# Optimization experiments

Hardware: AMD Instinct MI355X
Metric: run time of the kernel (lower is better)

## Reference

```python
import jax, jax.numpy as jnp
import numpy as np

N = 4096
F_IN = 512
F_OUT = 64
HEADS = 8
ALPHA = 0.2  # LeakyReLU negative slope
NEG_INF = -9e15


def setup_inputs() -> dict:
    key = jax.random.key(0)
    k1, k2, k3, k4 = jax.random.split(key, 4)
    x = jax.random.normal(k1, (N, F_IN), dtype=jnp.float32)
    adj = jax.random.randint(k2, (N, N), 0, 2, dtype=jnp.int32)  # dense 0/1 adjacency
    # xavier_uniform with gain=1.414 per head
    limW = 1.414 * float(np.sqrt(6.0 / (F_IN + F_OUT)))
    lima = 1.414 * float(np.sqrt(6.0 / (2 * F_OUT + 1)))
    W = jax.random.uniform(k3, (HEADS, F_IN, F_OUT), minval=-limW, maxval=limW, dtype=jnp.float32)
    a = jax.random.uniform(k4, (HEADS, 2 * F_OUT), minval=-lima, maxval=lima, dtype=jnp.float32)
    return {"x": x, "adj": adj, "W": W, "a": a}


def reference(x, adj, W, a):
    # Per-head linear: Wh [H, N, F_OUT]
    Wh = jnp.einsum("nf,hfo->hno", x, W)
    # Pairwise concat + matmul with a decomposes into f1_i + f2_j
    f1 = jnp.einsum("hno,ho->hn", Wh, a[:, :F_OUT])  # [H, N]
    f2 = jnp.einsum("hno,ho->hn", Wh, a[:, F_OUT:])  # [H, N]
    e = jax.nn.leaky_relu(f1[:, :, None] + f2[:, None, :], ALPHA)  # [H, N, N]
    e = jnp.where(adj[None, :, :] > 0, e, NEG_INF)
    attn = jax.nn.softmax(e, axis=-1)  # masked row softmax; dropout is eval-mode identity
    out = jnp.einsum("hnm,hmo->hno", attn, Wh)  # weighted aggregation
    # concat heads: [N, H*F_OUT]
    return jnp.transpose(out, (1, 0, 2)).reshape(N, HEADS * F_OUT)
```

## Files before the change

### kernel.cpp

```cpp
#include <hip/hip_runtime.h>
#include <hip/hip_bf16.h>

#define NN   4096
#define FIN  512
#define FOUT 64
#define NH   8
#define ALPHA 0.2f
#define ROWS 128
#define LOG2E 1.4426950408889634f

typedef __attribute__((ext_vector_type(8))) short bf16x8;
typedef __attribute__((ext_vector_type(4))) float f32x4;

__device__ __forceinline__ unsigned short f2bf(float x) {
    unsigned u = __float_as_uint(x);
    return (unsigned short)((u + 0x7fffu + ((u >> 16) & 1u)) >> 16);
}

__device__ __forceinline__ unsigned pk2(float a, float b) {
    union { __hip_bfloat162 h2; unsigned u; } cv;
    cv.h2 = __float22bfloat162_rn(float2{a, b});
    return cv.u;
}

__global__ __launch_bounds__(256) void kb(const int* __restrict__ adj,
                                          unsigned long long* __restrict__ bits) {
    const int wv   = blockIdx.x * 4 + (threadIdx.x >> 6);
    const int lane = threadIdx.x & 63;
    const int base = wv * 32;
    #pragma unroll
    for (int r = 0; r < 4; ++r) {
        int v0 = adj[(size_t)(base + r*8 + 0) * 64 + lane];
        int v1 = adj[(size_t)(base + r*8 + 1) * 64 + lane];
        int v2 = adj[(size_t)(base + r*8 + 2) * 64 + lane];
        int v3 = adj[(size_t)(base + r*8 + 3) * 64 + lane];
        int v4 = adj[(size_t)(base + r*8 + 4) * 64 + lane];
        int v5 = adj[(size_t)(base + r*8 + 5) * 64 + lane];
        int v6 = adj[(size_t)(base + r*8 + 6) * 64 + lane];
        int v7 = adj[(size_t)(base + r*8 + 7) * 64 + lane];
        unsigned long long m0 = __ballot(v0 > 0);
        unsigned long long m1 = __ballot(v1 > 0);
        unsigned long long m2 = __ballot(v2 > 0);
        unsigned long long m3 = __ballot(v3 > 0);
        unsigned long long m4 = __ballot(v4 > 0);
        unsigned long long m5 = __ballot(v5 > 0);
        unsigned long long m6 = __ballot(v6 > 0);
        unsigned long long m7 = __ballot(v7 > 0);
        if (lane == 0) {
            ulonglong2* dst = (ulonglong2*)&bits[base + r*8];
            dst[0] = {m0, m1};
            dst[1] = {m2, m3};
            dst[2] = {m4, m5};
            dst[3] = {m6, m7};
        }
    }
}

__global__ __launch_bounds__(256) void kg(const float* __restrict__ x,
                                          const float* __restrict__ W,
                                          const float* __restrict__ aw,
                                          unsigned short* __restrict__ WhTs,
                                          float* __restrict__ f1,
                                          float* __restrict__ f2) {
    __shared__ float As[16][68];
    __shared__ float Bs[16][68];
    __shared__ unsigned short Tb[64][80];
    __shared__ float r1[64][16];
    __shared__ float r2[64][16];
    const int t = threadIdx.x;
    const int bx   = blockIdx.x;
    const int h    = bx >> 6;
    const int nti  = bx & 63;
    const int row0 = nti * 64;
    const int tr = t >> 4, tc = t & 15;
    const int ar = t >> 2, ak = t & 3;
    const int bk = t >> 4, bo = t & 15;
    const float* WH = W + (size_t)h * FIN * FOUT;
    float acc[4][4] = {};

    for (int k0i = 0; k0i < FIN; k0i += 16) {
        __syncthreads();
        float4 av = *(const float4*)&x[(size_t)(row0 + ar) * FIN + k0i + ak * 4];
        As[ak*4+0][ar] = av.x; As[ak*4+1][ar] = av.y;
        As[ak*4+2][ar] = av.z; As[ak*4+3][ar] = av.w;
        *(float4*)&Bs[bk][bo*4] =
            *(const float4*)&WH[(size_t)(k0i + bk) * FOUT + bo*4];
        __syncthreads();
        #pragma unroll
        for (int kk = 0; kk < 16; ++kk) {
            float4 a4 = *(const float4*)&As[kk][tr*4];
            float4 b4 = *(const float4*)&Bs[kk][tc*4];
            float a[4] = {a4.x, a4.y, a4.z, a4.w};
            float b[4] = {b4.x, b4.y, b4.z, b4.w};
            #pragma unroll
            for (int i = 0; i < 4; ++i)
                #pragma unroll
                for (int j = 0; j < 4; ++j)
                    acc[i][j] = fmaf(a[i], b[j], acc[i][j]);
        }
    }

    float a1v[4], a2v[4];
    #pragma unroll
    for (int j = 0; j < 4; ++j) {
        a1v[j] = aw[h * 2 * FOUT + tc*4 + j];
        a2v[j] = aw[h * 2 * FOUT + FOUT + tc*4 + j];
    }
    #pragma unroll
    for (int i = 0; i < 4; ++i) {
        float s1 = 0.f, s2 = 0.f;
        #pragma unroll
        for (int j = 0; j < 4; ++j) {
            s1 = fmaf(acc[i][j], a1v[j], s1);
            s2 = fmaf(acc[i][j], a2v[j], s2);
            Tb[tc*4 + j][tr*4 + i] = f2bf(acc[i][j]);
        }
        r1[tr*4 + i][tc] = s1;
        r2[tr*4 + i][tc] = s2;
    }
    __syncthreads();
    if (t < 64) {
        float s1 = 0.f, s2 = 0.f;
        #pragma unroll
        for (int k = 0; k < 16; ++k) { s1 += r1[t][k]; s2 += r2[t][k]; }
        f1[h * NN + row0 + t] = s1 * LOG2E;
        f2[h * NN + row0 + t] = s2 * LOG2E;
    }
    unsigned char* tileB = (unsigned char*)(WhTs + ((size_t)(h * 64) + nti) * 4096);
    #pragma unroll
    for (int i = 0; i < 2; ++i) {
        int c = t + i * 256;
        int o = c >> 3, nch = c & 7;
        *(uint4*)(tileB + o * 128 + ((nch * 16) ^ ((o & 7) << 4))) =
            *(const uint4*)&Tb[o][nch * 8];
    }
}

__global__ __launch_bounds__(256, 4) void k3_attn(
        const unsigned long long* __restrict__ bits,
        const unsigned short* __restrict__ WhTs,
        const float* __restrict__ f1, const float* __restrict__ f2,
        float* __restrict__ pnum, float* __restrict__ pden) {
    __shared__ unsigned char psB[ROWS * 128];
    __shared__ unsigned char wsB[8192];
    const int t    = threadIdx.x;
    const int lane = t & 63, wid = t >> 6;
    const int h    = blockIdx.y;
    const int row0 = blockIdx.x * ROWS;
    const int js   = blockIdx.z, JS = gridDim.z;
    const int ntile = (NN / 64) / JS;
    const int nt0   = js * ntile;
    const int pr   = t >> 1, psub = t & 1;
    const float f1r = f1[h * NN + row0 + pr];
    const float* f2h = f2 + h * NN;
    const unsigned long long* bitsRow = bits + (size_t)(row0 + pr) * 64;
    const unsigned short* WTS = WhTs + (size_t)h * 64 * 4096;
    const int prswz = (pr & 7) << 4;
    f32x4 acc[2][4] = {};
    f32x4 accd[2] = {};
    const bf16x8 ones = {0x3F80, 0x3F80, 0x3F80, 0x3F80,
                         0x3F80, 0x3F80, 0x3F80, 0x3F80};

    uint4 wreg0, wreg1;
    auto loadW = [&](int nti, uint4& w0, uint4& w1) {
        const uint4* gt = (const uint4*)(WTS + (size_t)nti * 4096);
        w0 = gt[t];
        w1 = gt[t + 256];
    };
    loadW(nt0, wreg0, wreg1);

    const int kb2 = (lane >> 4) * 16;
    for (int it = 0; it < ntile; ++it) {
        const int nti = nt0 + it;
        __syncthreads();
        *(uint4*)&wsB[t * 16]        = wreg0;
        *(uint4*)&wsB[t * 16 + 4096] = wreg1;
        {
            unsigned msk = (unsigned)(bitsRow[nti] >> (psub << 5));
            const float* f2c = f2h + nti * 64 + psub * 32;
            #pragma unroll
            for (int q = 0; q < 4; ++q) {
                unsigned pk[4];
                #pragma unroll
                for (int c2 = 0; c2 < 2; ++c2) {
                    float4 f4 = *(const float4*)&f2c[q * 8 + c2 * 4];
                    float e0 = f1r + f4.x, e1 = f1r + f4.y;
                    float e2 = f1r + f4.z, e3 = f1r + f4.w;
                    e0 = fmaxf(e0, ALPHA * e0); e1 = fmaxf(e1, ALPHA * e1);
                    e2 = fmaxf(e2, ALPHA * e2); e3 = fmaxf(e3, ALPHA * e3);
                    const int b = q * 8 + c2 * 4;
                    float p0 = ((msk >> (b+0)) & 1u) ? __builtin_amdgcn_exp2f(e0) : 0.f;
                    float p1 = ((msk >> (b+1)) & 1u) ? __builtin_amdgcn_exp2f(e1) : 0.f;
                    float p2 = ((msk >> (b+2)) & 1u) ? __builtin_amdgcn_exp2f(e2) : 0.f;
                    float p3 = ((msk >> (b+3)) & 1u) ? __builtin_amdgcn_exp2f(e3) : 0.f;
                    pk[c2*2+0] = pk2(p0, p1);
                    pk[c2*2+1] = pk2(p2, p3);
                }
                uint4 w = {pk[0], pk[1], pk[2], pk[3]};
                *(uint4*)&psB[pr * 128 + ((psub*64 + q*16) ^ prswz)] = w;
            }
        }
        if (it + 1 < ntile) loadW(nti + 1, wreg0, wreg1);
        __syncthreads();
        #pragma unroll
        for (int fg = 0; fg < 2; ++fg) {
            const int arw  = wid * 32 + fg * 16 + (lane & 15);
            const int aswz = (arw & 7) << 4;
            #pragma unroll
            for (int ks = 0; ks < 2; ++ks) {
                bf16x8 af = *(const bf16x8*)&psB[arw * 128 + ((ks*64 + kb2) ^ aswz)];
                accd[fg] = __builtin_amdgcn_mfma_f32_16x16x32_bf16(af, ones, accd[fg], 0, 0, 0);
                #pragma unroll
                for (int cf = 0; cf < 4; ++cf) {
                    int brw = cf * 16 + (lane & 15);
                    bf16x8 bfr = *(const bf16x8*)&wsB[brw * 128 + ((ks*64 + kb2) ^ ((brw & 7) << 4))];
                    acc[fg][cf] = __builtin_amdgcn_mfma_f32_16x16x32_bf16(af, bfr, acc[fg][cf], 0, 0, 0);
                }
            }
        }
    }

    float* pn = pnum + (((size_t)js * NH + h) * NN + row0) * 64;
    #pragma unroll
    for (int fg = 0; fg < 2; ++fg)
        #pragma unroll
        for (int cf = 0; cf < 4; ++cf) {
            int o = cf * 16 + (lane & 15);
            #pragma unroll
            for (int rg = 0; rg < 4; ++rg) {
                int rl = wid * 32 + fg * 16 + (lane >> 4) * 4 + rg;
                pn[(size_t)rl * 64 + o] = acc[fg][cf][rg];
            }
        }
    if ((lane & 15) == 0) {
        float* pd = pden + ((size_t)js * NH + h) * NN + row0;
        #pragma unroll
        for (int fg = 0; fg < 2; ++fg)
            #pragma unroll
            for (int rg = 0; rg < 4; ++rg)
                pd[wid * 32 + fg * 16 + (lane >> 4) * 4 + rg] = accd[fg][rg];
    }
}

__global__ __launch_bounds__(256) void k4_red(const float* __restrict__ pnum,
                                              const float* __restrict__ pden,
                                              float* __restrict__ out, int JS) {
    const int idx = blockIdx.x * 256 + threadIdx.x;
    const int h   = idx >> 16;
    const int rem = idx & 65535;
    const int n   = rem >> 4;
    const int o4  = (rem & 15) * 4;
    float4 s = {0.f, 0.f, 0.f, 0.f};
    float  d = 0.f;
    for (int js = 0; js < JS; ++js) {
        const float* p = pnum + (((size_t)js * NH + h) * NN + n) * 64 + o4;
        float4 v = *(const float4*)p;
        s.x += v.x; s.y += v.y; s.z += v.z; s.w += v.w;
        d += pden[((size_t)js * NH + h) * NN + n];
    }
    float inv = 1.0f / d;
    float4 r = {s.x * inv, s.y * inv, s.z * inv, s.w * inv};
    *(float4*)&out[(size_t)n * (NH * FOUT) + h * FOUT + o4] = r;
}

extern "C" void kernel_launch(void* const* d_in, const int* in_sizes, int n_in,
                              void* d_out, int out_size, void* d_ws, size_t ws_size,
                              hipStream_t stream) {
    const float* x   = (const float*)d_in[0];
    const int*   adj = (const int*)d_in[1];
    const float* W   = (const float*)d_in[2];
    const float* a   = (const float*)d_in[3];
    float* outp = (float*)d_out;

    unsigned short* WhTs = (unsigned short*)d_ws;
    float* f1 = (float*)(WhTs + (size_t)NH * 64 * NN);
    float* f2 = f1 + NH * NN;
    unsigned long long* bits = (unsigned long long*)(f2 + NH * NN);
    float* pnum = (float*)(bits + (size_t)NN * 64);
    const size_t baseBytes  = (size_t)(pnum - (float*)d_ws) * 4;
    const size_t sliceBytes = (size_t)NH * NN * 65 * 4;
    int JS = 1;
    if (ws_size >= baseBytes + 4 * sliceBytes) JS = 4;
    else if (ws_size >= baseBytes + 2 * sliceBytes) JS = 2;
    float* pden = pnum + (size_t)JS * NH * NN * 64;

    kb     <<<dim3(2048),            256, 0, stream>>>(adj, bits);
    kg     <<<dim3(512),             256, 0, stream>>>(x, W, a, WhTs, f1, f2);
    k3_attn<<<dim3(NN/ROWS, NH, JS), 256, 0, stream>>>(bits, WhTs, f1, f2, pnum, pden);
    k4_red <<<dim3(NN*NH*FOUT/4/256), 256, 0, stream>>>(pnum, pden, outp, JS);
}
```

Baseline: 109.6 us.

## Use bf16 MFMA for the Wh projection with a pre-transposed bf16 W

Replaces the scalar fp32 shared-memory GEMM in kg with bf16 MFMA 16x16x32 instructions. A new small kernel kw first converts W to bf16 and transposes it so each lane can load contiguous 8-element B fragments. x is converted to bf16 on the fly and read directly from global memory without LDS staging. This adds one extra kernel launch and lowers the projection precision to bf16 inputs, which also affects f1/f2.

```diff
diff --git a/kernel.cpp b/kernel.cpp
--- a/kernel.cpp
+++ b/kernel.cpp
@@ -21,6 +21,10 @@
     union { __hip_bfloat162 h2; unsigned u; } cv;
     cv.h2 = __float22bfloat162_rn(float2{a, b});
     return cv.u;
+}
+
+__device__ __forceinline__ bf16x8 u4bf8(uint4 u) {
+    union { uint4 a; bf16x8 b; } cv; cv.a = u; return cv.b;
 }
 
 __global__ __launch_bounds__(256) void kb(const int* __restrict__ adj,
@@ -56,67 +60,81 @@
     }
 }
 
+__global__ __launch_bounds__(256) void kw(const float* __restrict__ W,
+                                          unsigned short* __restrict__ WT) {
+    __shared__ unsigned short T[64][72];
+    const int t  = threadIdx.x;
+    const int h  = blockIdx.x >> 3;
+    const int k0 = (blockIdx.x & 7) * 64;
+    #pragma unroll
+    for (int i = 0; i < 4; ++i) {
+        int idx = t + i * 256;
+        int kk = idx >> 4, o4 = (idx & 15) * 4;
+        float4 v = *(const float4*)&W[((size_t)h * FIN + k0 + kk) * FOUT + o4];
+        T[o4+0][kk] = f2bf(v.x); T[o4+1][kk] = f2bf(v.y);
+        T[o4+2][kk] = f2bf(v.z); T[o4+3][kk] = f2bf(v.w);
+    }
+    __syncthreads();
+    #pragma unroll
+    for (int i = 0; i < 2; ++i) {
+        int c = t + i * 256;
+        int o = c >> 3, kch = (c & 7) * 8;
+        *(uint4*)&WT[((size_t)h * 64 + o) * FIN + k0 + kch] =
+            *(const uint4*)&T[o][kch];
+    }
+}
+
 __global__ __launch_bounds__(256) void kg(const float* __restrict__ x,
-                                          const float* __restrict__ W,
+                                          const unsigned short* __restrict__ WT,
                                           const float* __restrict__ aw,
                                           unsigned short* __restrict__ WhTs,
                                           float* __restrict__ f1,
                                           float* __restrict__ f2) {
-    __shared__ float As[16][68];
-    __shared__ float Bs[16][68];
     __shared__ unsigned short Tb[64][80];
     __shared__ float r1[64][16];
     __shared__ float r2[64][16];
-    const int t = threadIdx.x;
-    const int bx   = blockIdx.x;
-    const int h    = bx >> 6;
-    const int nti  = bx & 63;
+    const int t = threadIdx.x, lane = t & 63, wid = t >> 6;
+    const int h    = blockIdx.x >> 6;
+    const int nti  = blockIdx.x & 63;
     const int row0 = nti * 64;
-    const int tr = t >> 4, tc = t & 15;
-    const int ar = t >> 2, ak = t & 3;
-    const int bk = t >> 4, bo = t & 15;
-    const float* WH = W + (size_t)h * FIN * FOUT;
-    float acc[4][4] = {};
-
-    for (int k0i = 0; k0i < FIN; k0i += 16) {
-        __syncthreads();
-        float4 av = *(const float4*)&x[(size_t)(row0 + ar) * FIN + k0i + ak * 4];
-        As[ak*4+0][ar] = av.x; As[ak*4+1][ar] = av.y;
-        As[ak*4+2][ar] = av.z; As[ak*4+3][ar] = av.w;
-        *(float4*)&Bs[bk][bo*4] =
-            *(const float4*)&WH[(size_t)(k0i + bk) * FOUT + bo*4];
-        __syncthreads();
-        #pragma unroll
-        for (int kk = 0; kk < 16; ++kk) {
-            float4 a4 = *(const float4*)&As[kk][tr*4];
-            float4 b4 = *(const float4*)&Bs[kk][tc*4];
-            float a[4] = {a4.x, a4.y, a4.z, a4.w};
-            float b[4] = {b4.x, b4.y, b4.z, b4.w};
-            #pragma unroll
-            for (int i = 0; i < 4; ++i)
-                #pragma unroll
-                for (int j = 0; j < 4; ++j)
-                    acc[i][j] = fmaf(a[i], b[j], acc[i][j]);
+    const int lrow = wid * 16 + (lane & 15);
+    const int kc   = (lane >> 4) * 8;
+    const float* xr = x + (size_t)(row0 + lrow) * FIN;
+    const unsigned short* WTh = WT + (size_t)h * 64 * FIN;
+    f32x4 acc[4] = {};
+
+    #pragma unroll 4
+    for (int k0 = 0; k0 < FIN; k0 += 32) {
+        float4 xa = *(const float4*)&xr[k0 + kc];
+        float4 xb = *(const float4*)&xr[k0 + kc + 4];
+        bf16x8 af = u4bf8(uint4{pk2(xa.x, xa.y), pk2(xa.z, xa.w),
+                                pk2(xb.x, xb.y), pk2(xb.z, xb.w)});
+        #pragma unroll
+        for (int cf = 0; cf < 4; ++cf) {
+            int o = cf * 16 + (lane & 15);
+            bf16x8 bfr = *(const bf16x8*)&WTh[(size_t)o * FIN + k0 + kc];
+            acc[cf] = __builtin_amdgcn_mfma_f32_16x16x32_bf16(af, bfr, acc[cf], 0, 0, 0);
         }
     }
 
     float a1v[4], a2v[4];
     #pragma unroll
-    for (int j = 0; j < 4; ++j) {
-        a1v[j] = aw[h * 2 * FOUT + tc*4 + j];
-        a2v[j] = aw[h * 2 * FOUT + FOUT + tc*4 + j];
-    }
-    #pragma unroll
-    for (int i = 0; i < 4; ++i) {
+    for (int cf = 0; cf < 4; ++cf) {
+        a1v[cf] = aw[h * 2 * FOUT + cf * 16 + (lane & 15)];
+        a2v[cf] = aw[h * 2 * FOUT + FOUT + cf * 16 + (lane & 15)];
+    }
+    #pragma unroll
+    for (int rg = 0; rg < 4; ++rg) {
+        const int lr = wid * 16 + (lane >> 4) * 4 + rg;
         float s1 = 0.f, s2 = 0.f;
         #pragma unroll
-        for (int j = 0; j < 4; ++j) {
-            s1 = fmaf(acc[i][j], a1v[j], s1);
-            s2 = fmaf(acc[i][j], a2v[j], s2);
-            Tb[tc*4 + j][tr*4 + i] = f2bf(acc[i][j]);
-        }
-        r1[tr*4 + i][tc] = s1;
-        r2[tr*4 + i][tc] = s2;
+        for (int cf = 0; cf < 4; ++cf) {
+            s1 = fmaf(acc[cf][rg], a1v[cf], s1);
+            s2 = fmaf(acc[cf][rg], a2v[cf], s2);
+            Tb[cf * 16 + (lane & 15)][lr] = f2bf(acc[cf][rg]);
+        }
+        r1[lr][lane & 15] = s1;
+        r2[lr][lane & 15] = s2;
     }
     __syncthreads();
     if (t < 64) {
@@ -275,9 +293,10 @@
     unsigned short* WhTs = (unsigned short*)d_ws;
     float* f1 = (float*)(WhTs + (size_t)NH * 64 * NN);
     float* f2 = f1 + NH * NN;
-    unsigned long long* bits = (unsigned long long*)(f2 + NH * NN);
+    unsigned short* WT = (unsigned short*)(f2 + NH * NN);
+    unsigned long long* bits = (unsigned long long*)(WT + (size_t)NH * 64 * FIN);
     float* pnum = (float*)(bits + (size_t)NN * 64);
-    const size_t baseBytes  = (size_t)(pnum - (float*)d_ws) * 4;
+    const size_t baseBytes  = (size_t)((char*)pnum - (char*)d_ws);
     const size_t sliceBytes = (size_t)NH * NN * 65 * 4;
     int JS = 1;
     if (ws_size >= baseBytes + 4 * sliceBytes) JS = 4;
@@ -285,7 +304,8 @@
     float* pden = pnum + (size_t)JS * NH * NN * 64;
 
     kb     <<<dim3(2048),            256, 0, stream>>>(adj, bits);
-    kg     <<<dim3(512),             256, 0, stream>>>(x, W, a, WhTs, f1, f2);
+    kw     <<<dim3(64),              256, 0, stream>>>(W, WT);
+    kg     <<<dim3(512),             256, 0, stream>>>(x, WT, a, WhTs, f1, f2);
     k3_attn<<<dim3(NN/ROWS, NH, JS), 256, 0, stream>>>(bits, WhTs, f1, f2, pnum, pden);
     k4_red <<<dim3(NN*NH*FOUT/4/256), 256, 0, stream>>>(pnum, pden, outp, JS);
 }
```

Measured after the change: 100.3 us. 8.5% less time.
